# Kernel tuning notes

Hardware: AMD Instinct MI355X
Metric: run time of the kernel (lower is better)

The kernel has to match this reference:

```python
import jax, jax.numpy as jnp
import numpy as np

B, NQ, NKV, QD, KVD, AD = 8, 4096, 4096, 1024, 1024, 128

def setup_inputs() -> dict:
    key = jax.random.key(0)
    ks = jax.random.split(key, 6)
    scale = lambda d: 1.0 / np.sqrt(d)
    return {
        "q": jax.random.normal(ks[0], (B, NQ, QD), dtype=jnp.float32),
        "k": jax.random.normal(ks[1], (B, NKV, KVD), dtype=jnp.float32),
        "v": jax.random.normal(ks[2], (B, NKV, KVD), dtype=jnp.float32),
        "Wq": jax.random.normal(ks[3], (QD, AD), dtype=jnp.float32) * scale(QD),
        "Wk": jax.random.normal(ks[4], (KVD, AD), dtype=jnp.float32) * scale(KVD),
        "Wv": jax.random.normal(ks[5], (KVD, AD), dtype=jnp.float32) * scale(KVD),
    }

def reference(q, k, v, Wq, Wk, Wv):
    s = AD ** (-0.5)
    Q = jnp.einsum('bnd,de->bne', q, Wq)   # [B,NQ,AD]
    K = jnp.einsum('bmd,de->bme', k, Wk)   # [B,NKV,AD]
    V = jnp.einsum('bmd,de->bme', v, Wv)   # [B,NKV,AD]
    sc = jnp.einsum('bne,bme->bnm', Q, K) * s  # [B,NQ,NKV]
    att = jax.nn.softmax(sc, axis=-1)
    return jnp.einsum('bnm,bme->bne', att, V)
```

## Files before the change

### kernel.cpp

```cpp
#include <hip/hip_runtime.h>
#include <cstdint>
#include <cstddef>

typedef __bf16 bf16_t;
typedef __bf16 bf16x8 __attribute__((ext_vector_type(8)));
typedef __bf16 bf16x4v __attribute__((ext_vector_type(4)));
typedef float f32x16 __attribute__((ext_vector_type(16)));

static __device__ __forceinline__ f32x16 mfma32(bf16x8 a, bf16x8 b, f32x16 c) {
  return __builtin_amdgcn_mfma_f32_32x32x16_bf16(a, b, c, 0, 0, 0);
}

static __device__ __forceinline__ void gld_lds16(const void* g, void* l) {
  __builtin_amdgcn_global_load_lds(
      (const __attribute__((address_space(1))) unsigned int*)g,
      (__attribute__((address_space(3))) unsigned int*)l, 16, 0, 0);
}

#define CEXP_CONST 0.12754582f


__global__ void wt_kernel(const float* __restrict__ Wq, const float* __restrict__ Wk,
                          const float* __restrict__ Wv, bf16_t* __restrict__ Wt2) {
  int t = blockIdx.x * 256 + threadIdx.x;
  int tensor = t >> 17;
  int r = t & 131071;
  int j = r & 7, l31 = (r >> 3) & 31, h = (r >> 8) & 1, nf = (r >> 9) & 3, k16 = (r >> 11) & 63;
  int k = k16 * 16 + h * 8 + j, n = nf * 32 + l31;
  const float* W = tensor == 0 ? Wq : (tensor == 1 ? Wk : Wv);
  Wt2[t] = (bf16_t)W[(size_t)k * 128 + n];
}

__global__ __launch_bounds__(256, 4) void proj_kernel(
    const float* __restrict__ xq, const float* __restrict__ xk, const float* __restrict__ xv,
    const bf16_t* __restrict__ WtAll,
    bf16_t* __restrict__ Qp, bf16_t* __restrict__ Kp, bf16_t* __restrict__ Vt) {
  __shared__ __align__(16) char smc[16384];
  const int tid = threadIdx.x;
  const int ty = blockIdx.y;
  const int bm = blockIdx.x;
  const float* X = (ty == 0) ? xq : (ty == 1) ? xk : xv;
  const bf16_t* W2 = WtAll + (size_t)ty * 131072;
  const int lane = tid & 63;
  const int w = tid >> 6;
  const int l31 = lane & 31, h = lane >> 5;

  const char* aG = (const char*)X + (size_t)bm * 131072;

  float4 S0[4], S1[4];
  auto ldg = [&](float4 (&S)[4], int p) {
#pragma unroll
    for (int i = 0; i < 4; ++i) {
      int c = i * 256 + tid;
      S[i] = *(const float4*)(aG + (size_t)(c >> 5) * 4096 + p * 512 + (c & 31) * 16);
    }
  };
  auto stg = [&](float4 (&S)[4], int buf) {
#pragma unroll
    for (int i = 0; i < 4; ++i) {
      int c = i * 256 + tid;
      int row = c >> 5, s = c & 31;
      bf16x4v bv;
      bv[0] = (bf16_t)S[i].x; bv[1] = (bf16_t)S[i].y;
      bv[2] = (bf16_t)S[i].z; bv[3] = (bf16_t)S[i].w;
      int dst = buf * 8192 + row * 256 + ((((s >> 1) ^ (row & 7)) << 4)) + (s & 1) * 8;
      *(uint2*)(smc + dst) = __builtin_bit_cast(uint2, bv);
    }
  };

  f32x16 acc;
#pragma unroll
  for (int r = 0; r < 16; ++r) acc[r] = 0.0f;
  const bf16_t* wbase = W2 + w * 512 + lane * 8;
  const int asw = l31 & 7;
  const char* arow0 = smc + l31 * 256;

  auto kloop = [&](int p) {
    const char* arow = arow0 + (p & 1) * 8192;
    const bf16_t* wp = wbase + (size_t)(p * 8) * 2048;
#pragma unroll
    for (int kk = 0; kk < 8; ++kk) {
      bf16x8 af = *(const bf16x8*)(arow + (((kk * 2 + h) ^ asw) << 4));
      bf16x8 wf = *(const bf16x8*)(wp + (size_t)kk * 2048);
      acc = mfma32(af, wf, acc);
    }
  };

  ldg(S0, 0);
  ldg(S1, 1);
  stg(S0, 0);
  ldg(S0, 2);
  __syncthreads();

#pragma unroll
  for (int p2 = 0; p2 < 4; ++p2) {
    {
      const int p = 2 * p2;
      kloop(p);
      __builtin_amdgcn_s_barrier();
      stg(S1, 1);
      if (p + 3 < 8) ldg(S1, p + 3);
      asm volatile("s_waitcnt lgkmcnt(0)" ::: "memory");
      __builtin_amdgcn_s_barrier();
    }
    {
      const int p = 2 * p2 + 1;
      kloop(p);
      __builtin_amdgcn_s_barrier();
      if (p < 7) {
        stg(S0, 0);
        if (p + 3 < 8) ldg(S0, p + 3);
        asm volatile("s_waitcnt lgkmcnt(0)" ::: "memory");
      }
      __builtin_amdgcn_s_barrier();
    }
  }
  __syncthreads();

  if (ty < 2) {
    constexpr int RS = 264;
#pragma unroll
    for (int r = 0; r < 16; ++r) {
      int m = (r & 3) + 8 * (r >> 2) + 4 * h;
      *(bf16_t*)(smc + m * RS + (w * 32 + l31) * 2) = (bf16_t)acc[r];
    }
    __syncthreads();
    bf16_t* O = (ty == 0) ? Qp : Kp;
    char* obase = (char*)O + (size_t)bm * 8192;
#pragma unroll
    for (int i = 0; i < 2; ++i) {
      int c = i * 256 + tid;
      int rr = c >> 4, ch = c & 15;
      uint4 vv = *(const uint4*)(smc + rr * RS + ch * 16);
      *(uint4*)(obase + rr * 256 + ch * 16) = vv;
    }
  } else {
#pragma unroll
    for (int q = 0; q < 4; ++q) {
      int n = w * 32 + l31;
      bf16x4v bv;
#pragma unroll
      for (int j = 0; j < 4; ++j) bv[j] = (bf16_t)acc[q * 4 + j];
      *(uint2*)(smc + n * 72 + q * 16 + h * 8) = __builtin_bit_cast(uint2, bv);
    }
    __syncthreads();
    const int bb = bm >> 7;
    const int m0 = (bm & 127) * 32;
    {
      int n = tid >> 1, half = tid & 1;
      const char* src = smc + n * 72 + half * 32;
      char* dst = (char*)Vt + (size_t)bb * 1048576 + (size_t)n * 8192 + m0 * 2 + half * 32;
      uint4 v0 = *(const uint4*)(src);
      uint4 v1 = *(const uint4*)(src + 16);
      *(uint4*)(dst) = v0;
      *(uint4*)(dst + 16) = v1;
    }
  }
}

template <int B0>
static __device__ __forceinline__ bf16x8 build_pf(const f32x16& s, int h) {
  unsigned c0, c1, c2, c3;
  asm("v_cvt_pk_bf16_f32 %0, %1, %2" : "=v"(c0) : "v"(s[B0 + 0]), "v"(s[B0 + 1]));
  asm("v_cvt_pk_bf16_f32 %0, %1, %2" : "=v"(c1) : "v"(s[B0 + 2]), "v"(s[B0 + 3]));
  asm("v_cvt_pk_bf16_f32 %0, %1, %2" : "=v"(c2) : "v"(s[B0 + 4]), "v"(s[B0 + 5]));
  asm("v_cvt_pk_bf16_f32 %0, %1, %2" : "=v"(c3) : "v"(s[B0 + 6]), "v"(s[B0 + 7]));
  unsigned x0 = (unsigned)__shfl_xor((int)c0, 32);
  unsigned x1 = (unsigned)__shfl_xor((int)c1, 32);
  unsigned x2 = (unsigned)__shfl_xor((int)c2, 32);
  unsigned x3 = (unsigned)__shfl_xor((int)c3, 32);
  uint4 u;
  u.x = h ? x2 : c0;
  u.y = h ? x3 : c1;
  u.z = h ? c2 : x0;
  u.w = h ? c3 : x1;
  return __builtin_bit_cast(bf16x8, u);
}

template <int SPLIT>
__global__ __launch_bounds__(256, 2) void attn_kernel(
    const bf16_t* __restrict__ Qp, const bf16_t* __restrict__ Kp,
    const bf16_t* __restrict__ Vt, float* __restrict__ out,
    float* __restrict__ Opart, float* __restrict__ Mpart, float* __restrict__ Lpart) {
  __shared__ __align__(16) char smc[65536];
  const int tid = threadIdx.x;
  const int lane = tid & 63, w = tid >> 6;
  const int l31 = lane & 31, h = lane >> 5;
  const int bid = blockIdx.x;
  const int b = bid & 7;
  const int qt = (bid >> 3) & 31;
  const int s = bid >> 8;
  const int NT = 64 / SPLIT;
  const float CEXP = CEXP_CONST;
  const int qbase = qt * 128 + w * 32;
  const int sw0 = (l31 ^ (l31 >> 3)) & 7;
  const int sw1 = sw0 ^ 4;

  bf16x8 qf[8];
  const bf16_t* qrow = Qp + (size_t)(b * 4096 + qbase + l31) * 128 + h * 8;
#pragma unroll
  for (int db = 0; db < 8; ++db) qf[db] = *(const bf16x8*)(qrow + db * 16);

  int swv[4];
#pragma unroll
  for (int nf = 0; nf < 4; ++nf) swv[nf] = (l31 & 7) ^ ((4 * nf + (l31 >> 3)) & 7);

  const int rl = lane >> 4, slK = lane & 15;
  const int dl = lane >> 3, slV = lane & 7;
  int koff[4], voff[4];
#pragma unroll
  for (int i = 0; i < 4; ++i) {
    int r = w * 16 + i * 4 + rl;
    int swr = (r ^ (r >> 3)) & 7;
    koff[i] = r * 256 + (((slK & 8) | ((slK & 7) ^ swr)) << 4);
    int d = w * 32 + i * 8 + dl;
    int swd = (d ^ (d >> 3)) & 7;
    voff[i] = d * 8192 + ((slV ^ swd) << 4);
  }
  const char* kpb = (const char*)Kp + (size_t)b * 1048576 + (size_t)s * NT * 16384;
  const char* vpb = (const char*)Vt + (size_t)b * 1048576 + (size_t)s * NT * 128;

  f32x16 oacc[4];
#pragma unroll
  for (int nf = 0; nf < 4; ++nf)
#pragma unroll
    for (int r = 0; r < 16; ++r) oacc[nf][r] = 0.0f;
  float m_run = -3.0e38f, lacc = 0.0f;

  auto stage = [&](int tt, int bufb) {
    const char* kb = kpb + (size_t)tt * 16384;
    const char* vb = vpb + (size_t)tt * 128;
    char* lk = smc + bufb + w * 4096;
    char* lv = smc + bufb + 16384 + w * 4096;
#pragma unroll
    for (int i = 0; i < 4; ++i) {
      gld_lds16(kb + koff[i], lk + i * 1024);
      gld_lds16(vb + voff[i], lv + i * 1024);
    }
  };

  stage(0, 0);
  stage(1, 32768);

  for (int t = 0; t < NT; ++t) {
    asm volatile("s_waitcnt vmcnt(8)" ::: "memory");
    __builtin_amdgcn_s_barrier();
    const char* kb = smc + (t & 1) * 32768;
    const char* vb = kb + 16384;

    f32x16 s0, s1;
#pragma unroll
    for (int i = 0; i < 16; ++i) { s0[i] = 0.0f; s1[i] = 0.0f; }
    __builtin_amdgcn_s_setprio(1);
#pragma unroll
    for (int db = 0; db < 8; ++db) {
      const int q = 2 * db + h;
      bf16x8 k0 = *(const bf16x8*)(kb + l31 * 256 + (((q & 8) | ((q & 7) ^ sw0)) << 4));
      bf16x8 k1 = *(const bf16x8*)(kb + (32 + l31) * 256 + (((q & 8) | ((q & 7) ^ sw1)) << 4));
      s0 = mfma32(k0, qf[db], s0);
      s1 = mfma32(k1, qf[db], s1);
    }
    __builtin_amdgcn_s_setprio(0);

    float tmax = fmaxf(s0[0], s1[0]);
#pragma unroll
    for (int i = 1; i < 16; ++i) tmax = fmaxf(tmax, fmaxf(s0[i], s1[i]));
    tmax = fmaxf(tmax, __shfl_xor(tmax, 32));
    if (__any(tmax > m_run + 62.0f)) {
      float mnew = fmaxf(m_run, tmax);
      float fac = exp2f((m_run - mnew) * CEXP);
      m_run = mnew;
      lacc *= fac;
#pragma unroll
      for (int r = 0; r < 16; ++r) {
        float fr = __shfl(fac, (r & 3) + 8 * (r >> 2) + 4 * h);
#pragma unroll
        for (int nf = 0; nf < 4; ++nf) oacc[nf][r] *= fr;
      }
    }
    const float mc = m_run * CEXP;
#pragma unroll
    for (int i = 0; i < 16; ++i) s0[i] = exp2f(fmaf(s0[i], CEXP, -mc));
#pragma unroll
    for (int i = 0; i < 16; ++i) s1[i] = exp2f(fmaf(s1[i], CEXP, -mc));
    float a0 = 0.f, a1 = 0.f, a2 = 0.f, a3 = 0.f;
#pragma unroll
    for (int i = 0; i < 16; i += 4) {
      a0 += s0[i] + s1[i];         a1 += s0[i + 1] + s1[i + 1];
      a2 += s0[i + 2] + s1[i + 2]; a3 += s0[i + 3] + s1[i + 3];
    }
    lacc += (a0 + a1) + (a2 + a3);

    __builtin_amdgcn_s_setprio(1);
    {
      bf16x8 pf = build_pf<0>(s0, h);
#pragma unroll
      for (int nf = 0; nf < 4; ++nf) {
        bf16x8 vf = *(const bf16x8*)(vb + (nf * 32 + l31) * 128 + (((0 + h) ^ swv[nf]) << 4));
        oacc[nf] = mfma32(pf, vf, oacc[nf]);
      }
    }
    {
      bf16x8 pf = build_pf<8>(s0, h);
#pragma unroll
      for (int nf = 0; nf < 4; ++nf) {
        bf16x8 vf = *(const bf16x8*)(vb + (nf * 32 + l31) * 128 + (((2 + h) ^ swv[nf]) << 4));
        oacc[nf] = mfma32(pf, vf, oacc[nf]);
      }
    }
    {
      bf16x8 pf = build_pf<0>(s1, h);
#pragma unroll
      for (int nf = 0; nf < 4; ++nf) {
        bf16x8 vf = *(const bf16x8*)(vb + (nf * 32 + l31) * 128 + (((4 + h) ^ swv[nf]) << 4));
        oacc[nf] = mfma32(pf, vf, oacc[nf]);
      }
    }
    {
      bf16x8 pf = build_pf<8>(s1, h);
#pragma unroll
      for (int nf = 0; nf < 4; ++nf) {
        bf16x8 vf = *(const bf16x8*)(vb + (nf * 32 + l31) * 128 + (((6 + h) ^ swv[nf]) << 4));
        oacc[nf] = mfma32(pf, vf, oacc[nf]);
      }
    }
    __builtin_amdgcn_s_setprio(0);

    __builtin_amdgcn_s_barrier();
    stage((t + 2) & (NT - 1), (t & 1) * 32768);
  }
  asm volatile("s_waitcnt vmcnt(0)" ::: "memory");

  lacc += __shfl_xor(lacc, 32);
  if (SPLIT == 1) {
    const float inv = 1.0f / lacc;
    float* ob = out + (size_t)(b * 4096 + qbase) * 128;
#pragma unroll
    for (int r = 0; r < 16; ++r) {
      const int rowD = (r & 3) + 8 * (r >> 2) + 4 * h;
      float ir = __shfl(inv, rowD);
#pragma unroll
      for (int nf = 0; nf < 4; ++nf)
        ob[(size_t)rowD * 128 + nf * 32 + l31] = oacc[nf][r] * ir;
    }
  } else {
    const int pb = s * 256 + b * 32 + qt;
    if (lane < 32) {
      Mpart[pb * 128 + w * 32 + l31] = m_run;
      Lpart[pb * 128 + w * 32 + l31] = lacc;
    }
    float* ob = Opart + ((size_t)pb * 128 + w * 32) * 128;
#pragma unroll
    for (int r = 0; r < 16; ++r) {
      const int rowD = (r & 3) + 8 * (r >> 2) + 4 * h;
#pragma unroll
      for (int nf = 0; nf < 4; ++nf)
        ob[(size_t)rowD * 128 + nf * 32 + l31] = oacc[nf][r];
    }
  }
}

__global__ __launch_bounds__(256) void combine_kernel(
    const float* __restrict__ Opart, const float* __restrict__ Mpart,
    const float* __restrict__ Lpart, float* __restrict__ out) {
  const int g = blockIdx.x * 8 + (threadIdx.x >> 5);
  const int lane32 = threadIdx.x & 31;
  const int b = g >> 12;
  const int pos = g & 4095;
  const int qt = pos >> 7;
  const int row = pos & 127;
  const int i0 = (b * 32 + qt) * 128 + row;
  const int i1 = (256 + b * 32 + qt) * 128 + row;
  const float m0 = Mpart[i0], m1 = Mpart[i1];
  const float l0 = Lpart[i0], l1 = Lpart[i1];
  const float m = fmaxf(m0, m1);
  const float w0 = exp2f((m0 - m) * CEXP_CONST);
  const float w1 = exp2f((m1 - m) * CEXP_CONST);
  const float inv = 1.0f / (w0 * l0 + w1 * l1);
  const float4 o0 = *(const float4*)(Opart + (size_t)i0 * 128 + lane32 * 4);
  const float4 o1 = *(const float4*)(Opart + (size_t)i1 * 128 + lane32 * 4);
  float4 o;
  o.x = (w0 * o0.x + w1 * o1.x) * inv;
  o.y = (w0 * o0.y + w1 * o1.y) * inv;
  o.z = (w0 * o0.z + w1 * o1.z) * inv;
  o.w = (w0 * o0.w + w1 * o1.w) * inv;
  *(float4*)(out + (size_t)g * 128 + lane32 * 4) = o;
}

extern "C" void kernel_launch(void* const* d_in, const int* in_sizes, int n_in,
                              void* d_out, int out_size, void* d_ws, size_t ws_size,
                              hipStream_t stream) {
  const float* q  = (const float*)d_in[0];
  const float* k  = (const float*)d_in[1];
  const float* v  = (const float*)d_in[2];
  const float* Wq = (const float*)d_in[3];
  const float* Wk = (const float*)d_in[4];
  const float* Wv = (const float*)d_in[5];
  float* out = (float*)d_out;
  char* ws = (char*)d_ws;
  bf16_t* Wt2 = (bf16_t*)(ws);
  bf16_t* Qp = (bf16_t*)(ws + (size_t)(1u << 20));
  bf16_t* Kp = (bf16_t*)(ws + (size_t)(9u << 20));
  bf16_t* Vt = (bf16_t*)(ws + (size_t)(17u << 20));
  float* Opart = (float*)(ws + (size_t)(32u << 20));
  float* Mpart = (float*)(ws + (size_t)(64u << 20));
  float* Lpart = (float*)(ws + (size_t)(64u << 20) + (256u << 10));

  hipLaunchKernelGGL(wt_kernel, dim3(1536), dim3(256), 0, stream, Wq, Wk, Wv, Wt2);
  hipLaunchKernelGGL(proj_kernel, dim3(1024, 3), dim3(256), 0, stream, q, k, v, Wt2, Qp, Kp, Vt);

  if (ws_size >= ((size_t)65 << 20)) {
    hipLaunchKernelGGL((attn_kernel<2>), dim3(512), dim3(256), 0, stream,
                       Qp, Kp, Vt, out, Opart, Mpart, Lpart);
    hipLaunchKernelGGL(combine_kernel, dim3(4096), dim3(256), 0, stream,
                       Opart, Mpart, Lpart, out);
  } else {
    hipLaunchKernelGGL((attn_kernel<1>), dim3(256), dim3(256), 0, stream,
                       Qp, Kp, Vt, out, Opart, Mpart, Lpart);
  }
}
```

Baseline: 209.9 us.

## Prefetch weight fragments into registers and cut input staging to one buffer

The projection kernel now loads the next K-chunk's weight fragments into a second register set (wA/wB ping-pong) before running the MFMA loop on the current chunk. Previously those weights were loaded inline inside the MFMA loop. It also drops one of the two float4 staging register sets for the input rows. Each step now uses one __syncthreads instead of two explicit barriers with waits. The intent is to hide global weight-load latency and reduce synchronization, at the cost of 16 extra bf16x8 registers per thread with launch_bounds(256,4) occupancy.

Measured after the change: 206.5 us (median of 2 runs). No clear change (-1.6%).

```diff
diff --git a/kernel.cpp b/kernel.cpp
--- a/kernel.cpp
+++ b/kernel.cpp
@@ -47,15 +47,15 @@
 
   const char* aG = (const char*)X + (size_t)bm * 131072;
 
-  float4 S0[4], S1[4];
-  auto ldg = [&](float4 (&S)[4], int p) {
+  float4 S[4];
+  auto ldg = [&](int p) {
 #pragma unroll
     for (int i = 0; i < 4; ++i) {
       int c = i * 256 + tid;
       S[i] = *(const float4*)(aG + (size_t)(c >> 5) * 4096 + p * 512 + (c & 31) * 16);
     }
   };
-  auto stg = [&](float4 (&S)[4], int buf) {
+  auto stg = [&](int buf) {
 #pragma unroll
     for (int i = 0; i < 4; ++i) {
       int c = i * 256 + tid;
@@ -68,54 +68,50 @@
     }
   };
 
+  bf16x8 wA[8], wB[8];
+  const bf16_t* wbase = W2 + w * 512 + lane * 8;
+  auto ldw = [&](bf16x8 (&Wf)[8], int p) {
+#pragma unroll
+    for (int kk = 0; kk < 8; ++kk)
+      Wf[kk] = *(const bf16x8*)(wbase + (size_t)(p * 8 + kk) * 2048);
+  };
+
   f32x16 acc;
 #pragma unroll
   for (int r = 0; r < 16; ++r) acc[r] = 0.0f;
-  const bf16_t* wbase = W2 + w * 512 + lane * 8;
   const int asw = l31 & 7;
-  const char* arow0 = smc + l31 * 256;
-
-  auto kloop = [&](int p) {
-    const char* arow = arow0 + (p & 1) * 8192;
-    const bf16_t* wp = wbase + (size_t)(p * 8) * 2048;
+  auto kloop = [&](bf16x8 (&Wf)[8], int buf) {
+    const char* arow = smc + buf * 8192 + l31 * 256;
 #pragma unroll
     for (int kk = 0; kk < 8; ++kk) {
       bf16x8 af = *(const bf16x8*)(arow + (((kk * 2 + h) ^ asw) << 4));
-      bf16x8 wf = *(const bf16x8*)(wp + (size_t)kk * 2048);
-      acc = mfma32(af, wf, acc);
+      acc = mfma32(af, Wf[kk], acc);
     }
   };
 
-  ldg(S0, 0);
-  ldg(S1, 1);
-  stg(S0, 0);
-  ldg(S0, 2);
+  ldg(0);
+  stg(0);
+  ldg(1);
+  ldw(wA, 0);
   __syncthreads();
 
 #pragma unroll
   for (int p2 = 0; p2 < 4; ++p2) {
-    {
-      const int p = 2 * p2;
-      kloop(p);
-      __builtin_amdgcn_s_barrier();
-      stg(S1, 1);
-      if (p + 3 < 8) ldg(S1, p + 3);
-      asm volatile("s_waitcnt lgkmcnt(0)" ::: "memory");
-      __builtin_amdgcn_s_barrier();
-    }
-    {
-      const int p = 2 * p2 + 1;
-      kloop(p);
-      __builtin_amdgcn_s_barrier();
-      if (p < 7) {
-        stg(S0, 0);
-        if (p + 3 < 8) ldg(S0, p + 3);
-        asm volatile("s_waitcnt lgkmcnt(0)" ::: "memory");
-      }
-      __builtin_amdgcn_s_barrier();
-    }
-  }
-  __syncthreads();
+    const int pe = 2 * p2;
+    ldw(wB, pe + 1);
+    kloop(wA, 0);
+    stg(1);
+    if (pe + 2 < 8) ldg(pe + 2);
+    __syncthreads();
+    const int po = pe + 1;
+    if (po + 1 < 8) ldw(wA, po + 1);
+    kloop(wB, 1);
+    if (po + 1 < 8) {
+      stg(0);
+      if (po + 2 < 8) ldg(po + 2);
+    }
+    __syncthreads();
+  }
 
   if (ty < 2) {
     constexpr int RS = 264;
```
